# Kernel tuning notes

Hardware: AMD Instinct MI355X
Metric: run time of the kernel (lower is better)

Reference implementation:

```python
import jax, jax.numpy as jnp
import numpy as np

N, D = 768, 64
EPS = 1e-5

def _ln(x, g, b):
    u = x.mean(-1, keepdims=True)
    s = ((x - u) ** 2).mean(-1, keepdims=True)
    return g * (x - u) / jnp.sqrt(s + EPS) + b

def setup_inputs() -> dict:
    key = jax.random.key(0)
    ks = jax.random.split(key, 16)
    inp = {
        'corr_index': jax.random.normal(ks[0], (N, N, 2), dtype=jnp.float32),
        'nei_index': jax.random.randint(ks[1], (N, N), 0, 2, dtype=jnp.int32),
        'nei_num': jax.random.randint(ks[2], (N,), 0, N, dtype=jnp.int32),
        'hidden_state': jax.random.normal(ks[3], (N, D), dtype=jnp.float32),
        'cn': jax.random.normal(ks[4], (N, D), dtype=jnp.float32),
        # relativeLayer: MLP(2 -> D)
        'W_r': jax.random.normal(ks[5], (2, D)) * 0.01, 'b_r': jnp.zeros((D,)),
        'g_r': jnp.ones((D,)), 'be_r': jax.random.normal(ks[6], (D,)) * 0.02,
        # ngate: MLP_gate(3D -> D)
        'W_g': jax.random.normal(ks[7], (3 * D, D)) * 0.01, 'b_g': jnp.zeros((D,)),
        'g_g': jnp.ones((D,)), 'be_g': jax.random.normal(ks[8], (D,)) * 0.02,
        # WAr: MLP(3D -> 1)
        'W_a': jax.random.normal(ks[9], (3 * D, 1)) * 0.01, 'b_a': jnp.zeros((1,)),
        'g_a': jnp.ones((1,)), 'be_a': jnp.abs(jax.random.normal(ks[10], (1,))) * 0.02 + 0.01,
        # weight: MLP(D -> D)
        'W_w': jax.random.normal(ks[11], (D, D)) * 0.01, 'b_w': jnp.zeros((D,)),
        'g_w': jnp.ones((D,)), 'be_w': jax.random.normal(ks[12], (D,)) * 0.02,
    }
    return inp

def reference(corr_index, nei_index, nei_num, hidden_state, cn,
              W_r, b_r, g_r, be_r, W_g, b_g, g_g, be_g,
              W_a, b_a, g_a, be_a, W_w, b_w, g_w, be_w):
    n, d = hidden_state.shape
    mask = nei_index > 0  # [N,N]; (i,j): j is neighbor of i
    # relativeLayer on all pairs (values at masked positions match the torch gather)
    r = jax.nn.relu(_ln(corr_index @ W_r + b_r, g_r, be_r))  # [N,N,D]
    hi = jnp.broadcast_to(hidden_state[:, None, :], (n, n, d))  # hi_t: h[i]
    hj = jnp.broadcast_to(hidden_state[None, :, :], (n, n, d))  # nei_inputs: h[j]
    tmp = jnp.concatenate([r, hi, hj], axis=-1)  # [N,N,3D]
    nGate = jax.nn.sigmoid(_ln(tmp @ W_g + b_g, g_g, be_g))  # [N,N,D]
    tt = jax.nn.relu(_ln(tmp @ W_a + b_a, g_a, be_a))[..., 0]  # [N,N]
    Pos = jnp.where(mask, tt, 0.0)
    Pos = jnp.where(Pos == 0.0, -10000.0, Pos)  # Pos[Pos==0] = -10000
    Pos = jax.nn.softmax(Pos, axis=1)  # masked row-softmax over neighbors j
    # H[i,j] = h[j] * nGate[i,j] * Pos[i,j] at masked pairs, else 0
    H = jnp.where(mask[..., None], hj * nGate * Pos[..., None], 0.0)
    H_sum = jax.nn.relu(_ln(jnp.sum(H, axis=1) @ W_w + b_w, g_w, be_w))  # [N,D]
    C = H_sum + cn
    H_out = hidden_state + jnp.tanh(C)
    return (H_out, C)
```

## Files before the change

kernel.cpp:

```cpp
#include <hip/hip_runtime.h>


#define NN 768
#define DD 64
#define EPSF 1e-5f
#define LOG2E 1.44269504f

typedef __attribute__((ext_vector_type(8))) short short8;
typedef __attribute__((ext_vector_type(4))) float float4v;
typedef __attribute__((ext_vector_type(2))) float float2v;

__device__ __forceinline__ unsigned short f2bf(float f) {
  unsigned int u = __float_as_uint(f);
  u += 0x7fffu + ((u >> 16) & 1u);
  return (unsigned short)(u >> 16);
}

__device__ __forceinline__ float fast_tanh(float x) {
  float e = __builtin_amdgcn_exp2f(fminf(x, 20.f) * (2.f * LOG2E));
  return (e - 1.f) * __builtin_amdgcn_rcpf(e + 1.f);
}

__global__ __launch_bounds__(256) void prep_kernel(
    const float* __restrict__ hidden, const float* __restrict__ Wg,
    const float* __restrict__ bg, const float* __restrict__ Wr,
    const float* __restrict__ br, const float* __restrict__ gr,
    const float* __restrict__ ber, const float* __restrict__ gg,
    const float* __restrict__ beg, float* __restrict__ A_pre,
    float2v* __restrict__ BH, float4v* __restrict__ KT,
    float2v* __restrict__ GB, float* __restrict__ evec,
    unsigned short* __restrict__ WgT) {
  const int bid = blockIdx.x;
  const int tid = threadIdx.x;

  if (bid == NN / 4) {
    for (int idx = tid; idx < DD * DD; idx += 256) {
      int n = idx >> 6, k = idx & 63;
      WgT[idx] = f2bf(Wg[k * DD + n]);
    }
    if (tid < 64) {
      int t = tid;
      float w0 = Wr[t], w1 = Wr[DD + t], bb = br[t];
      float m0 = w0, m1 = w1, mb = bb;
      for (int m = 1; m < 64; m <<= 1) {
        m0 += __shfl_xor(m0, m);
        m1 += __shfl_xor(m1, m);
        mb += __shfl_xor(mb, m);
      }
      m0 *= (1.f / DD);
      m1 *= (1.f / DD);
      mb *= (1.f / DD);
      float a0 = w0 - m0, a1 = w1 - m1, ab = bb - mb;
      float grt = gr[t];
      float4v kt;
      kt[0] = grt * a0;
      kt[1] = grt * a1;
      kt[2] = grt * ab;
      kt[3] = ber[t];
      KT[t] = kt;
      float2v gb;
      gb[0] = -LOG2E * gg[t];
      gb[1] = -LOG2E * beg[t];
      GB[t] = gb;
      float e00 = a0 * a0, e11 = a1 * a1, ebb = ab * ab;
      float e01 = a0 * a1, e0b = a0 * ab, e1b = a1 * ab;
      for (int m = 1; m < 64; m <<= 1) {
        e00 += __shfl_xor(e00, m);
        e11 += __shfl_xor(e11, m);
        ebb += __shfl_xor(ebb, m);
        e01 += __shfl_xor(e01, m);
        e0b += __shfl_xor(e0b, m);
        e1b += __shfl_xor(e1b, m);
      }
      if (t == 0) {
        evec[0] = e00 * (1.f / DD);
        evec[1] = e11 * (1.f / DD);
        evec[2] = ebb * (1.f / DD);
        evec[3] = e01 * (1.f / DD);
        evec[4] = e0b * (1.f / DD);
        evec[5] = e1b * (1.f / DD);
      }
    }
    return;
  }

  const int w = tid >> 6;
  const int lane = tid & 63;
  const int i = bid * 4 + w;
  float hv = hidden[i * DD + lane];
  float a = bg[lane];
  float b = 0.f;
#pragma unroll 8
  for (int k = 0; k < DD; ++k) {
    float hk = __shfl(hv, k);
    a = fmaf(hk, Wg[(DD + k) * DD + lane], a);
    b = fmaf(hk, Wg[(2 * DD + k) * DD + lane], b);
  }
  A_pre[i * DD + lane] = a;
  float2v bh2;
  bh2[0] = b;
  bh2[1] = hv;
  BH[i * DD + lane] = bh2;
}

__global__ __launch_bounds__(512, 4) void gat_kernel(
    const int* __restrict__ nei, const float2v* __restrict__ corr2,
    const float* __restrict__ A_pre, const float2v* __restrict__ BH,
    const float4v* __restrict__ KT, const float2v* __restrict__ GB,
    const float* __restrict__ evec, const unsigned short* __restrict__ WgT,
    const float* __restrict__ hidden, const float* __restrict__ cn,
    const float* __restrict__ bea, const float* __restrict__ Ww,
    const float* __restrict__ bw, const float* __restrict__ gw,
    const float* __restrict__ bew, float* __restrict__ out) {
  __shared__ __align__(16) unsigned short Rt[8][16 * 72];
  __shared__ short Lst[NN];
  __shared__ float red[8][DD];
  __shared__ int cLds;

  const int i = blockIdx.x;
  const int tid = threadIdx.x;
  const int wid = tid >> 6;
  const int lane = tid & 63;
  const int quad = lane >> 4;
  const int nl = lane & 15;
  const int p16 = lane & 15;

  if (tid == 0) cLds = 0;
  __syncthreads();
  {
    int jj = tid;
    if (nei[i * NN + jj] > 0) {
      int idx = atomicAdd(&cLds, 1);
      Lst[idx] = (short)jj;
    }
    jj = tid + 512;
    if (jj < NN && nei[i * NN + jj] > 0) {
      int idx = atomicAdd(&cLds, 1);
      Lst[idx] = (short)jj;
    }
  }
  __syncthreads();
  const int cnt = cLds;

  const float e00 = evec[0], e11 = evec[1], ebb = evec[2];
  const float e01 = evec[3], e0b = evec[4], e1b = evec[5];
  const float4v kt = KT[lane];

  short8 Bf[2][4];
#pragma unroll
  for (int ks = 0; ks < 2; ++ks)
#pragma unroll
    for (int nt = 0; nt < 4; ++nt)
      __builtin_memcpy(&Bf[ks][nt],
                       &WgT[(nt * 16 + nl) * DD + ks * 32 + quad * 8], 16);

  float ngg[4], nbeg[4], pre4[4];
#pragma unroll
  for (int nt = 0; nt < 4; ++nt) {
    int d = nt * 16 + nl;
    float2v gb = GB[d];
    ngg[nt] = gb[0];
    nbeg[nt] = gb[1];
    pre4[nt] = A_pre[i * DD + d];
  }

  float accT[4] = {0.f, 0.f, 0.f, 0.f};

  for (int base = wid * 16; base < cnt; base += 128) {
    int pg = base + p16;
    int jp = (int)Lst[pg < cnt ? pg : cnt - 1];
    float2v cc = corr2[i * NN + jp];
    float var = cc[0] * cc[0] * e00 + cc[1] * cc[1] * e11 + ebb +
                2.f * (cc[0] * cc[1] * e01 + cc[0] * e0b + cc[1] * e1b);
    float iv = __builtin_amdgcn_rsqf(var + EPSF);

#pragma unroll
    for (int q = 0; q < 16; ++q) {
      float sc0 = __shfl(cc[0], q);
      float sc1 = __shfl(cc[1], q);
      float siv = __shfl(iv, q);
      float s3 = fmaf(sc0, kt[0], fmaf(sc1, kt[1], kt[2]));
      float r = fmaxf(0.f, fmaf(siv, s3, kt[3]));
      Rt[wid][q * 72 + lane] = f2bf(r);
    }
    __builtin_amdgcn_fence(__ATOMIC_ACQ_REL, "workgroup");

    int jpr[4];
    float pv[4];
#pragma unroll
    for (int rr = 0; rr < 4; ++rr) {
      int pl = quad * 4 + rr;
      jpr[rr] = __shfl(jp, pl);
      pv[rr] = (base + pl < cnt) ? 1.f : 0.f;
    }
    float2v bh2[4][4];
#pragma unroll
    for (int rr = 0; rr < 4; ++rr)
#pragma unroll
      for (int nt = 0; nt < 4; ++nt)
        bh2[rr][nt] = BH[jpr[rr] * DD + nt * 16 + nl];

    short8 a0, a1;
    __builtin_memcpy(&a0, &Rt[wid][nl * 72 + quad * 8], 16);
    __builtin_memcpy(&a1, &Rt[wid][nl * 72 + 32 + quad * 8], 16);
    float4v acc[4];
#pragma unroll
    for (int nt = 0; nt < 4; ++nt) {
      float4v z = {0.f, 0.f, 0.f, 0.f};
      z = __builtin_amdgcn_mfma_f32_16x16x32_bf16(a0, Bf[0][nt], z, 0, 0, 0);
      z = __builtin_amdgcn_mfma_f32_16x16x32_bf16(a1, Bf[1][nt], z, 0, 0, 0);
      acc[nt] = z;
    }

    float y[4][4];
#pragma unroll
    for (int nt = 0; nt < 4; ++nt)
#pragma unroll
      for (int rr = 0; rr < 4; ++rr)
        y[nt][rr] = acc[nt][rr] + pre4[nt] + bh2[rr][nt][0];
#pragma unroll
    for (int rr = 0; rr < 4; ++rr) {
      float s = y[0][rr] + y[1][rr] + y[2][rr] + y[3][rr];
      float qq = y[0][rr] * y[0][rr] + y[1][rr] * y[1][rr] +
                 y[2][rr] * y[2][rr] + y[3][rr] * y[3][rr];
#pragma unroll
      for (int m = 1; m < 16; m <<= 1) {
        s += __shfl_xor(s, m);
        qq += __shfl_xor(qq, m);
      }
      float u = s * (1.f / DD);
      float vv = qq * (1.f / DD) - u * u;
      float inv = __builtin_amdgcn_rsqf(vv + EPSF);
#pragma unroll
      for (int nt = 0; nt < 4; ++nt) {
        float e = __builtin_amdgcn_exp2f(fmaf(ngg[nt] * (y[nt][rr] - u), inv, nbeg[nt]));
        float gate = __builtin_amdgcn_rcpf(1.f + e);
        accT[nt] = fmaf(gate * pv[rr], bh2[rr][nt][1], accT[nt]);
      }
    }
  }

#pragma unroll
  for (int nt = 0; nt < 4; ++nt) {
    accT[nt] += __shfl_xor(accT[nt], 16);
    accT[nt] += __shfl_xor(accT[nt], 32);
  }
  if (lane < 16) {
#pragma unroll
    for (int nt = 0; nt < 4; ++nt) red[wid][nt * 16 + nl] = accT[nt];
  }
  __syncthreads();

  if (tid < 64) {
    const int d = tid;
    float hs = 0.f;
#pragma unroll
    for (int w = 0; w < 8; ++w) hs += red[w][d];
    float tta = fmaxf(bea[0], 0.f);
    float wgt = (tta > 0.f && cnt > 0) ? __builtin_amdgcn_rcpf((float)cnt)
                                       : (1.f / (float)NN);
    hs *= wgt;

    float dotv = bw[d];
#pragma unroll 8
    for (int k = 0; k < DD; ++k) {
      float hk = __shfl(hs, k);
      dotv = fmaf(hk, Ww[k * DD + d], dotv);
    }
    float s = dotv, qq = dotv * dotv;
#pragma unroll
    for (int m = 1; m < 64; m <<= 1) {
      s += __shfl_xor(s, m);
      qq += __shfl_xor(qq, m);
    }
    float u = s * (1.f / DD);
    float var2 = qq * (1.f / DD) - u * u;
    float inv = __builtin_amdgcn_rsqf(var2 + EPSF);
    float val = fmaxf(0.f, fmaf(gw[d], (dotv - u) * inv, bew[d]));
    float Cv = val + cn[i * DD + d];
    out[i * DD + d] = hidden[i * DD + d] + fast_tanh(Cv);
    out[NN * DD + i * DD + d] = Cv;
  }
}

extern "C" void kernel_launch(void* const* d_in, const int* in_sizes, int n_in,
                              void* d_out, int out_size, void* d_ws,
                              size_t ws_size, hipStream_t stream) {
  const float* corr = (const float*)d_in[0];
  const int* nei = (const int*)d_in[1];
  const float* hidden = (const float*)d_in[3];
  const float* cn = (const float*)d_in[4];
  const float* Wr = (const float*)d_in[5];
  const float* br = (const float*)d_in[6];
  const float* gr = (const float*)d_in[7];
  const float* ber = (const float*)d_in[8];
  const float* Wg = (const float*)d_in[9];
  const float* bg = (const float*)d_in[10];
  const float* gg = (const float*)d_in[11];
  const float* beg = (const float*)d_in[12];
  const float* bea = (const float*)d_in[16];
  const float* Ww = (const float*)d_in[17];
  const float* bw = (const float*)d_in[18];
  const float* gw = (const float*)d_in[19];
  const float* bew = (const float*)d_in[20];
  float* out = (float*)d_out;

  float* ws = (float*)d_ws;
  float* A_pre = ws;
  float2v* BH = (float2v*)(ws + 49152);
  float4v* KT = (float4v*)(ws + 147456);
  float2v* GB = (float2v*)(ws + 147712);
  float* evec = ws + 147840;
  unsigned short* WgT = (unsigned short*)(ws + 147856);

  prep_kernel<<<NN / 4 + 1, 256, 0, stream>>>(hidden, Wg, bg, Wr, br, gr, ber,
                                              gg, beg, A_pre, BH, KT, GB, evec,
                                              WgT);
  gat_kernel<<<NN, 512, 0, stream>>>((const int*)nei, (const float2v*)corr,
                                     A_pre, BH, KT, GB, evec, WgT, hidden, cn,
                                     bea, Ww, bw, gw, bew, out);
}
```

Before: 134.5 us.

## Precompute neighbor lists and compacted coords in prep; compute relu features in registers

Moves neighbor-list compaction out of the main kernel into 768 extra prep blocks, which also write compacted corr coordinates so the main kernel reads them contiguously. The main loop software-prefetches the next chunk's indices and coords, and builds the MFMA A-operand directly in registers from KT instead of staging it through LDS with shuffles. This removes LDS traffic, the block-wide barriers and the gather latency from gat_kernel. In exchange it adds global round-trips for the lists and more per-lane arithmetic and KT loads.

```diff
diff --git a/kernel.cpp b/kernel.cpp
--- a/kernel.cpp
+++ b/kernel.cpp
@@ -2,6 +2,7 @@
 
 
 #define NN 768
+#define NNP 784
 #define DD 64
 #define EPSF 1e-5f
 #define LOG2E 1.44269504f
@@ -9,6 +10,7 @@
 typedef __attribute__((ext_vector_type(8))) short short8;
 typedef __attribute__((ext_vector_type(4))) float float4v;
 typedef __attribute__((ext_vector_type(2))) float float2v;
+typedef __attribute__((ext_vector_type(4))) unsigned short ushort4v;
 
 __device__ __forceinline__ unsigned short f2bf(float f) {
   unsigned int u = __float_as_uint(f);
@@ -26,14 +28,45 @@
     const float* __restrict__ bg, const float* __restrict__ Wr,
     const float* __restrict__ br, const float* __restrict__ gr,
     const float* __restrict__ ber, const float* __restrict__ gg,
-    const float* __restrict__ beg, float* __restrict__ A_pre,
+    const float* __restrict__ beg, const int* __restrict__ nei,
+    const float2v* __restrict__ corr2, float* __restrict__ A_pre,
     float2v* __restrict__ BH, float4v* __restrict__ KT,
     float2v* __restrict__ GB, float* __restrict__ evec,
-    unsigned short* __restrict__ WgT) {
+    unsigned short* __restrict__ WgT, int* __restrict__ cnt_g,
+    unsigned short* __restrict__ Lst_g, float2v* __restrict__ Cc) {
   const int bid = blockIdx.x;
   const int tid = threadIdx.x;
 
-  if (bid == NN / 4) {
+  if (bid < NN) {
+    __shared__ short Lst[NN];
+    __shared__ int cLds;
+    if (tid == 0) cLds = 0;
+    __syncthreads();
+#pragma unroll
+    for (int rep = 0; rep < 3; ++rep) {
+      int jj = tid + rep * 256;
+      if (nei[bid * NN + jj] > 0) {
+        int idx = atomicAdd(&cLds, 1);
+        Lst[idx] = (short)jj;
+      }
+    }
+    __syncthreads();
+    const int cnt = cLds;
+    if (tid == 0) cnt_g[bid] = cnt;
+    for (int idx = tid; idx < cnt; idx += 256) {
+      int jp = (int)Lst[idx];
+      Lst_g[bid * NNP + idx] = (unsigned short)jp;
+      Cc[bid * NNP + idx] = corr2[bid * NN + jp];
+    }
+    if (cnt > 0 && tid < 16) {
+      int jp0 = (int)Lst[0];
+      Lst_g[bid * NNP + cnt + tid] = (unsigned short)jp0;
+      Cc[bid * NNP + cnt + tid] = corr2[bid * NN + jp0];
+    }
+    return;
+  }
+
+  if (bid == NN) {
     for (int idx = tid; idx < DD * DD; idx += 256) {
       int n = idx >> 6, k = idx & 63;
       WgT[idx] = f2bf(Wg[k * DD + n]);
@@ -86,7 +119,7 @@
 
   const int w = tid >> 6;
   const int lane = tid & 63;
-  const int i = bid * 4 + w;
+  const int i = (bid - NN - 1) * 4 + w;
   float hv = hidden[i * DD + lane];
   float a = bg[lane];
   float b = 0.f;
@@ -104,18 +137,16 @@
 }
 
 __global__ __launch_bounds__(512, 4) void gat_kernel(
-    const int* __restrict__ nei, const float2v* __restrict__ corr2,
     const float* __restrict__ A_pre, const float2v* __restrict__ BH,
     const float4v* __restrict__ KT, const float2v* __restrict__ GB,
     const float* __restrict__ evec, const unsigned short* __restrict__ WgT,
-    const float* __restrict__ hidden, const float* __restrict__ cn,
-    const float* __restrict__ bea, const float* __restrict__ Ww,
-    const float* __restrict__ bw, const float* __restrict__ gw,
-    const float* __restrict__ bew, float* __restrict__ out) {
-  __shared__ __align__(16) unsigned short Rt[8][16 * 72];
-  __shared__ short Lst[NN];
+    const int* __restrict__ cnt_g, const unsigned short* __restrict__ Lst_g,
+    const float2v* __restrict__ Cc, const float* __restrict__ hidden,
+    const float* __restrict__ cn, const float* __restrict__ bea,
+    const float* __restrict__ Ww, const float* __restrict__ bw,
+    const float* __restrict__ gw, const float* __restrict__ bew,
+    float* __restrict__ out) {
   __shared__ float red[8][DD];
-  __shared__ int cLds;
 
   const int i = blockIdx.x;
   const int tid = threadIdx.x;
@@ -123,28 +154,11 @@
   const int lane = tid & 63;
   const int quad = lane >> 4;
   const int nl = lane & 15;
-  const int p16 = lane & 15;
-
-  if (tid == 0) cLds = 0;
-  __syncthreads();
-  {
-    int jj = tid;
-    if (nei[i * NN + jj] > 0) {
-      int idx = atomicAdd(&cLds, 1);
-      Lst[idx] = (short)jj;
-    }
-    jj = tid + 512;
-    if (jj < NN && nei[i * NN + jj] > 0) {
-      int idx = atomicAdd(&cLds, 1);
-      Lst[idx] = (short)jj;
-    }
-  }
-  __syncthreads();
-  const int cnt = cLds;
+
+  const int cnt = cnt_g[i];
 
   const float e00 = evec[0], e11 = evec[1], ebb = evec[2];
   const float e01 = evec[3], e0b = evec[4], e1b = evec[5];
-  const float4v kt = KT[lane];
 
   short8 Bf[2][4];
 #pragma unroll
@@ -166,43 +180,47 @@
 
   float accT[4] = {0.f, 0.f, 0.f, 0.f};
 
-  for (int base = wid * 16; base < cnt; base += 128) {
-    int pg = base + p16;
-    int jp = (int)Lst[pg < cnt ? pg : cnt - 1];
-    float2v cc = corr2[i * NN + jp];
+  int base = wid * 16;
+  ushort4v l4 = {0, 0, 0, 0};
+  float2v cc = {0.f, 0.f};
+  if (base < cnt) {
+    __builtin_memcpy(&l4, &Lst_g[i * NNP + base + quad * 4], 8);
+    cc = Cc[i * NNP + base + nl];
+  }
+
+  for (; base < cnt; base += 128) {
+    const int nb = base + 128;
+    ushort4v l4n = {0, 0, 0, 0};
+    float2v ccn = {0.f, 0.f};
+    if (nb < cnt) {
+      __builtin_memcpy(&l4n, &Lst_g[i * NNP + nb + quad * 4], 8);
+      ccn = Cc[i * NNP + nb + nl];
+    }
+
+    int jpr[4] = {(int)l4[0], (int)l4[1], (int)l4[2], (int)l4[3]};
+    float2v bh2[4][4];
+#pragma unroll
+    for (int rr = 0; rr < 4; ++rr)
+#pragma unroll
+      for (int nt = 0; nt < 4; ++nt)
+        bh2[rr][nt] = BH[jpr[rr] * DD + nt * 16 + nl];
+
     float var = cc[0] * cc[0] * e00 + cc[1] * cc[1] * e11 + ebb +
                 2.f * (cc[0] * cc[1] * e01 + cc[0] * e0b + cc[1] * e1b);
     float iv = __builtin_amdgcn_rsqf(var + EPSF);
-
-#pragma unroll
-    for (int q = 0; q < 16; ++q) {
-      float sc0 = __shfl(cc[0], q);
-      float sc1 = __shfl(cc[1], q);
-      float siv = __shfl(iv, q);
-      float s3 = fmaf(sc0, kt[0], fmaf(sc1, kt[1], kt[2]));
-      float r = fmaxf(0.f, fmaf(siv, s3, kt[3]));
-      Rt[wid][q * 72 + lane] = f2bf(r);
-    }
-    __builtin_amdgcn_fence(__ATOMIC_ACQ_REL, "workgroup");
-
-    int jpr[4];
-    float pv[4];
-#pragma unroll
-    for (int rr = 0; rr < 4; ++rr) {
-      int pl = quad * 4 + rr;
-      jpr[rr] = __shfl(jp, pl);
-      pv[rr] = (base + pl < cnt) ? 1.f : 0.f;
-    }
-    float2v bh2[4][4];
-#pragma unroll
-    for (int rr = 0; rr < 4; ++rr)
-#pragma unroll
-      for (int nt = 0; nt < 4; ++nt)
-        bh2[rr][nt] = BH[jpr[rr] * DD + nt * 16 + nl];
+    float d0 = iv * cc[0], d1 = iv * cc[1];
 
     short8 a0, a1;
-    __builtin_memcpy(&a0, &Rt[wid][nl * 72 + quad * 8], 16);
-    __builtin_memcpy(&a1, &Rt[wid][nl * 72 + 32 + quad * 8], 16);
+#pragma unroll
+    for (int e = 0; e < 8; ++e) {
+      float4v k0 = KT[quad * 8 + e];
+      float4v k1 = KT[32 + quad * 8 + e];
+      float r0 = fmaxf(0.f, fmaf(d0, k0[0], fmaf(d1, k0[1], fmaf(iv, k0[2], k0[3]))));
+      float r1 = fmaxf(0.f, fmaf(d0, k1[0], fmaf(d1, k1[1], fmaf(iv, k1[2], k1[3]))));
+      a0[e] = (short)f2bf(r0);
+      a1[e] = (short)f2bf(r1);
+    }
+
     float4v acc[4];
 #pragma unroll
     for (int nt = 0; nt < 4; ++nt) {
@@ -212,6 +230,11 @@
       acc[nt] = z;
     }
 
+    float pv[4];
+#pragma unroll
+    for (int rr = 0; rr < 4; ++rr)
+      pv[rr] = (base + quad * 4 + rr < cnt) ? 1.f : 0.f;
+
     float y[4][4];
 #pragma unroll
     for (int nt = 0; nt < 4; ++nt)
@@ -233,11 +256,15 @@
       float inv = __builtin_amdgcn_rsqf(vv + EPSF);
 #pragma unroll
       for (int nt = 0; nt < 4; ++nt) {
-        float e = __builtin_amdgcn_exp2f(fmaf(ngg[nt] * (y[nt][rr] - u), inv, nbeg[nt]));
+        float e = __builtin_amdgcn_exp2f(
+            fmaf(ngg[nt] * (y[nt][rr] - u), inv, nbeg[nt]));
         float gate = __builtin_amdgcn_rcpf(1.f + e);
         accT[nt] = fmaf(gate * pv[rr], bh2[rr][nt][1], accT[nt]);
       }
     }
+
+    l4 = l4n;
+    cc = ccn;
   }
 
 #pragma unroll
@@ -312,11 +339,14 @@
   float2v* GB = (float2v*)(ws + 147712);
   float* evec = ws + 147840;
   unsigned short* WgT = (unsigned short*)(ws + 147856);
-
-  prep_kernel<<<NN / 4 + 1, 256, 0, stream>>>(hidden, Wg, bg, Wr, br, gr, ber,
-                                              gg, beg, A_pre, BH, KT, GB, evec,
-                                              WgT);
-  gat_kernel<<<NN, 512, 0, stream>>>((const int*)nei, (const float2v*)corr,
-                                     A_pre, BH, KT, GB, evec, WgT, hidden, cn,
-                                     bea, Ww, bw, gw, bew, out);
-}
+  int* cnt_g = (int*)(ws + 149904);
+  unsigned short* Lst_g = (unsigned short*)(ws + 150672);
+  float2v* Cc = (float2v*)(ws + 451728);
+
+  prep_kernel<<<NN + 1 + NN / 4, 256, 0, stream>>>(
+      hidden, Wg, bg, Wr, br, gr, ber, gg, beg, nei, (const float2v*)corr,
+      A_pre, BH, KT, GB, evec, WgT, cnt_g, Lst_g, Cc);
+  gat_kernel<<<NN, 512, 0, stream>>>(A_pre, BH, KT, GB, evec, WgT, cnt_g,
+                                     Lst_g, Cc, hidden, cn, bea, Ww, bw, gw,
+                                     bew, out);
+}
```

Result: slower. 169.6 us (+26.1%).

## Build MFMA A-fragments in registers and stage neighbor coords in LDS

Applied to the files above, without the earlier changes.

The relative-layer activations are now computed directly into the MFMA A-operand registers from KT coefficients held in LDS. This removes the per-tile shuffle loop, the LDS round-trip through the Rt scratch and its fence. Neighbor corr values are gathered into LDS during list compaction and the list is padded, so the main loop loads indices with one vector read and issues the BH gathers earlier. Each lane now does 16 relu evaluations instead of 16 shuffled ones, and an extra block barrier is added.

```diff
diff --git a/kernel.cpp b/kernel.cpp
--- a/kernel.cpp
+++ b/kernel.cpp
@@ -9,6 +9,7 @@
 typedef __attribute__((ext_vector_type(8))) short short8;
 typedef __attribute__((ext_vector_type(4))) float float4v;
 typedef __attribute__((ext_vector_type(2))) float float2v;
+typedef __attribute__((ext_vector_type(4))) unsigned short ushort4v;
 
 __device__ __forceinline__ unsigned short f2bf(float f) {
   unsigned int u = __float_as_uint(f);
@@ -112,8 +113,9 @@
     const float* __restrict__ bea, const float* __restrict__ Ww,
     const float* __restrict__ bw, const float* __restrict__ gw,
     const float* __restrict__ bew, float* __restrict__ out) {
-  __shared__ __align__(16) unsigned short Rt[8][16 * 72];
-  __shared__ short Lst[NN];
+  __shared__ unsigned short Lst[NN + 16];
+  __shared__ float2v CcL[NN + 16];
+  __shared__ float4v KTl[72];
   __shared__ float red[8][DD];
   __shared__ int cLds;
 
@@ -123,28 +125,33 @@
   const int lane = tid & 63;
   const int quad = lane >> 4;
   const int nl = lane & 15;
-  const int p16 = lane & 15;
 
   if (tid == 0) cLds = 0;
+  if (tid < 64) KTl[tid + (tid >> 3)] = KT[tid];
   __syncthreads();
   {
     int jj = tid;
     if (nei[i * NN + jj] > 0) {
       int idx = atomicAdd(&cLds, 1);
-      Lst[idx] = (short)jj;
+      Lst[idx] = (unsigned short)jj;
+      CcL[idx] = corr2[i * NN + jj];
     }
     jj = tid + 512;
     if (jj < NN && nei[i * NN + jj] > 0) {
       int idx = atomicAdd(&cLds, 1);
-      Lst[idx] = (short)jj;
+      Lst[idx] = (unsigned short)jj;
+      CcL[idx] = corr2[i * NN + jj];
     }
   }
   __syncthreads();
   const int cnt = cLds;
+  if (cnt > 0 && tid < 16) {
+    Lst[cnt + tid] = Lst[0];
+    CcL[cnt + tid] = CcL[0];
+  }
 
   const float e00 = evec[0], e11 = evec[1], ebb = evec[2];
   const float e01 = evec[3], e0b = evec[4], e1b = evec[5];
-  const float4v kt = KT[lane];
 
   short8 Bf[2][4];
 #pragma unroll
@@ -165,44 +172,41 @@
   }
 
   float accT[4] = {0.f, 0.f, 0.f, 0.f};
+  __syncthreads();
 
   for (int base = wid * 16; base < cnt; base += 128) {
-    int pg = base + p16;
-    int jp = (int)Lst[pg < cnt ? pg : cnt - 1];
-    float2v cc = corr2[i * NN + jp];
+    ushort4v l4;
+    __builtin_memcpy(&l4, &Lst[base + quad * 4], 8);
+    int jpr[4] = {(int)l4[0], (int)l4[1], (int)l4[2], (int)l4[3]};
+
+    float2v bh2[4][4];
+#pragma unroll
+    for (int rr = 0; rr < 4; ++rr)
+#pragma unroll
+      for (int nt = 0; nt < 4; ++nt)
+        bh2[rr][nt] = BH[jpr[rr] * DD + nt * 16 + nl];
+
+    float2v cc = CcL[base + nl];
     float var = cc[0] * cc[0] * e00 + cc[1] * cc[1] * e11 + ebb +
                 2.f * (cc[0] * cc[1] * e01 + cc[0] * e0b + cc[1] * e1b);
     float iv = __builtin_amdgcn_rsqf(var + EPSF);
-
-#pragma unroll
-    for (int q = 0; q < 16; ++q) {
-      float sc0 = __shfl(cc[0], q);
-      float sc1 = __shfl(cc[1], q);
-      float siv = __shfl(iv, q);
-      float s3 = fmaf(sc0, kt[0], fmaf(sc1, kt[1], kt[2]));
-      float r = fmaxf(0.f, fmaf(siv, s3, kt[3]));
-      Rt[wid][q * 72 + lane] = f2bf(r);
-    }
-    __builtin_amdgcn_fence(__ATOMIC_ACQ_REL, "workgroup");
-
-    int jpr[4];
-    float pv[4];
-#pragma unroll
-    for (int rr = 0; rr < 4; ++rr) {
-      int pl = quad * 4 + rr;
-      jpr[rr] = __shfl(jp, pl);
-      pv[rr] = (base + pl < cnt) ? 1.f : 0.f;
-    }
-    float2v bh2[4][4];
-#pragma unroll
-    for (int rr = 0; rr < 4; ++rr)
-#pragma unroll
-      for (int nt = 0; nt < 4; ++nt)
-        bh2[rr][nt] = BH[jpr[rr] * DD + nt * 16 + nl];
+    float d0 = iv * cc[0], d1 = iv * cc[1];
 
     short8 a0, a1;
-    __builtin_memcpy(&a0, &Rt[wid][nl * 72 + quad * 8], 16);
-    __builtin_memcpy(&a1, &Rt[wid][nl * 72 + 32 + quad * 8], 16);
+#pragma unroll
+    for (int e = 0; e < 8; ++e) {
+      int k0i = quad * 9 + e;
+      int k1i = 36 + quad * 9 + e;
+      float4v k0 = KTl[k0i];
+      float4v k1 = KTl[k1i];
+      float r0 =
+          fmaxf(0.f, fmaf(d0, k0[0], fmaf(d1, k0[1], fmaf(iv, k0[2], k0[3]))));
+      float r1 =
+          fmaxf(0.f, fmaf(d0, k1[0], fmaf(d1, k1[1], fmaf(iv, k1[2], k1[3]))));
+      a0[e] = (short)f2bf(r0);
+      a1[e] = (short)f2bf(r1);
+    }
+
     float4v acc[4];
 #pragma unroll
     for (int nt = 0; nt < 4; ++nt) {
@@ -212,6 +216,11 @@
       acc[nt] = z;
     }
 
+    float pv[4];
+#pragma unroll
+    for (int rr = 0; rr < 4; ++rr)
+      pv[rr] = (base + quad * 4 + rr < cnt) ? 1.f : 0.f;
+
     float y[4][4];
 #pragma unroll
     for (int nt = 0; nt < 4; ++nt)
@@ -233,7 +242,8 @@
       float inv = __builtin_amdgcn_rsqf(vv + EPSF);
 #pragma unroll
       for (int nt = 0; nt < 4; ++nt) {
-        float e = __builtin_amdgcn_exp2f(fmaf(ngg[nt] * (y[nt][rr] - u), inv, nbeg[nt]));
+        float e = __builtin_amdgcn_exp2f(
+            fmaf(ngg[nt] * (y[nt][rr] - u), inv, nbeg[nt]));
         float gate = __builtin_amdgcn_rcpf(1.f + e);
         accT[nt] = fmaf(gate * pv[rr], bh2[rr][nt][1], accT[nt]);
       }
```

After: 162.3 us. +20.7%, slower.
